# Optimization experiments

Hardware: AMD Instinct MI355X
Metric: run time of the kernel (lower is better)

The kernel has to match this reference:

```python
import jax, jax.numpy as jnp
import numpy as np

B, H, T, D = 2, 16, 2048, 64
R1, R2 = 4, 8


def setup_inputs() -> dict:
    key = jax.random.key(0)
    ks = jax.random.split(key, 7)
    return {
        "q": jax.random.normal(ks[0], (B, H, T, D), dtype=jnp.float32),
        "k": jax.random.normal(ks[1], (B, H, T, D), dtype=jnp.float32),
        "v": jax.random.normal(ks[2], (B, H, T, D), dtype=jnp.float32),
        "W_q": jax.random.normal(ks[3], (H, D, R1 * R2), dtype=jnp.float32) / np.sqrt(D),
        "W_k": jax.random.normal(ks[4], (H, D, R1 * R2), dtype=jnp.float32) / np.sqrt(D),
        "core1": jax.random.normal(ks[5], (H, R1), dtype=jnp.float32),
        "core2": jax.random.normal(ks[6], (H, R2), dtype=jnp.float32),
    }


def reference(q, k, v, W_q, W_k, core1, core2):
    """Kronecker low-rank (LSR) causal attention.

    scores[b,h,m,n] = (1/sqrt(R1*R2)) * sum_r kron[h,r] * (q@W_q)[b,h,m,r] * (k@W_k)[b,h,n,r]
    where kron[h] = core1[h] (x) core2[h]  (per-head Kronecker product).
    """
    Hh, r1 = core1.shape
    r2 = core2.shape[1]
    # per-head Kronecker core vector: (H, R1*R2)
    kron = (core1[:, :, None] * core2[:, None, :]).reshape(Hh, r1 * r2)
    scale = 1.0 / jnp.sqrt(jnp.float32(r1 * r2))
    # low-rank projections, rank R = R1*R2
    q_lr = jnp.einsum("bhtd,hdr->bhtr", q, W_q) * kron[None, :, None, :]  # [B,H,T,R]
    k_lr = jnp.einsum("bhtd,hdr->bhtr", k, W_k)                            # [B,H,T,R]
    scores = jnp.einsum("bhmr,bhnr->bhmn", q_lr, k_lr) * scale             # [B,H,T,T]
    t = q.shape[2]
    causal = jnp.tril(jnp.ones((t, t), dtype=bool))
    scores = jnp.where(causal[None, None], scores, -jnp.inf)
    p = jax.nn.softmax(scores, axis=-1)
    return jnp.einsum("bhmn,bhnd->bhmd", p, v)
```

## Files before the change

kernel.cpp:

```cpp
#include <hip/hip_runtime.h>

typedef _Float16 f16;
typedef _Float16 f16x2 __attribute__((ext_vector_type(2)));
typedef _Float16 f16x4 __attribute__((ext_vector_type(4)));
typedef _Float16 f16x8 __attribute__((ext_vector_type(8)));
typedef float    f32x4 __attribute__((ext_vector_type(4)));
typedef float    f32x16 __attribute__((ext_vector_type(16)));

constexpr int B_ = 2, H_ = 16, T_ = 2048, D_ = 64, R_ = 32, NT = 32;

__device__ __forceinline__ f32x4 mfma16(f16x8 a, f16x8 b, f32x4 c) {
  return __builtin_amdgcn_mfma_f32_16x16x32_f16(a, b, c, 0, 0, 0);
}
__device__ __forceinline__ f32x16 mfma32(f16x8 a, f16x8 b, f32x16 c) {
  return __builtin_amdgcn_mfma_f32_32x32x16_f16(a, b, c, 0, 0, 0);
}
__device__ __forceinline__ void ld_lds16(const void* g, void* l) {
  __builtin_amdgcn_global_load_lds(
      (const __attribute__((address_space(1))) unsigned int*)g,
      (__attribute__((address_space(3))) unsigned int*)l, 16, 0, 0);
}

__global__ __launch_bounds__(256) void proj_kernel(
    const float* __restrict__ q, const float* __restrict__ k, const float* __restrict__ v,
    const float* __restrict__ Wq, const float* __restrict__ Wk,
    const float* __restrict__ c1, const float* __restrict__ c2,
    f16* __restrict__ qlr, f16* __restrict__ klr, f16* __restrict__ vt)
{
  __shared__ float sv[64 * 65];

  const int tid = threadIdx.x, w = tid >> 6, lane = tid & 63;
  const int l15 = lane & 15, l4 = lane >> 4;
  const int bh = blockIdx.x >> 5, h = bh & (H_ - 1);
  const int t0 = (blockIdx.x & 31) * 64;

  const float* vb = v + ((size_t)bh * T_ + t0) * D_;
  float4 vld[4];
#pragma unroll
  for (int it = 0; it < 4; ++it) vld[it] = ((const float4*)vb)[it * 256 + tid];

  const int m = t0 + 16 * w + l15;
  const float* qr = q + ((size_t)bh * T_ + m) * D_;
  const float* kr = k + ((size_t)bh * T_ + m) * D_;
  f16x8 aq[2], ak[2];
#pragma unroll
  for (int kc = 0; kc < 2; ++kc) {
    float4 x0 = *(const float4*)(qr + kc * 32 + 8 * l4);
    float4 x1 = *(const float4*)(qr + kc * 32 + 8 * l4 + 4);
    float4 y0 = *(const float4*)(kr + kc * 32 + 8 * l4);
    float4 y1 = *(const float4*)(kr + kc * 32 + 8 * l4 + 4);
    f16x8 A, K;
    A[0]=(f16)x0.x; A[1]=(f16)x0.y; A[2]=(f16)x0.z; A[3]=(f16)x0.w;
    A[4]=(f16)x1.x; A[5]=(f16)x1.y; A[6]=(f16)x1.z; A[7]=(f16)x1.w;
    K[0]=(f16)y0.x; K[1]=(f16)y0.y; K[2]=(f16)y0.z; K[3]=(f16)y0.w;
    K[4]=(f16)y1.x; K[5]=(f16)y1.y; K[6]=(f16)y1.z; K[7]=(f16)y1.w;
    aq[kc] = A; ak[kc] = K;
  }

  const float* Wqh = Wq + (size_t)h * D_ * R_;
  const float* Wkh = Wk + (size_t)h * D_ * R_;
  f16x8 bq[2][2], bk[2][2];
#pragma unroll
  for (int kc = 0; kc < 2; ++kc)
#pragma unroll
    for (int nt = 0; nt < 2; ++nt) {
      const int r = 16 * nt + l15;
      f16x8 q8, k8;
#pragma unroll
      for (int j2 = 0; j2 < 8; ++j2) {
        const int d = kc * 32 + 8 * l4 + j2;
        q8[j2] = (f16)Wqh[d * R_ + r];
        k8[j2] = (f16)Wkh[d * R_ + r];
      }
      bq[kc][nt] = q8; bk[kc][nt] = k8;
    }

#pragma unroll
  for (int it = 0; it < 4; ++it) {
    const int i4 = it * 256 + tid, t = i4 >> 4, dq = (i4 & 15) * 4;
    sv[t * 65 + dq    ] = vld[it].x;
    sv[t * 65 + dq + 1] = vld[it].y;
    sv[t * 65 + dq + 2] = vld[it].z;
    sv[t * 65 + dq + 3] = vld[it].w;
  }

  const f32x4 z4 = {0.f, 0.f, 0.f, 0.f};
#pragma unroll
  for (int nt = 0; nt < 2; ++nt) {
    f32x4 accq = mfma16(aq[0], bq[0][nt], z4);
    accq = mfma16(aq[1], bq[1][nt], accq);
    f32x4 acck = mfma16(ak[0], bk[0][nt], z4);
    acck = mfma16(ak[1], bk[1][nt], acck);
    const int r = 16 * nt + l15;
    const float scl = c1[h * 4 + (r >> 3)] * c2[h * 8 + (r & 7)] *
                      (0.17677669529663687f * 1.4426950408889634f);
#pragma unroll
    for (int i = 0; i < 4; ++i) {
      const size_t row = (size_t)bh * T_ + t0 + 16 * w + 4 * l4 + i;
      qlr[row * R_ + r] = (f16)(accq[i] * scl);
      klr[row * R_ + r] = (f16)acck[i];
    }
  }

  __syncthreads();
#pragma unroll
  for (int it = 0; it < 8; ++it) {
    const int idx = it * 256 + tid, d = idx >> 5, t = (idx & 31) * 2;
    const float f0 = sv[t * 65 + d], f1 = sv[t * 65 + 65 + d];
    f16x2 pr; pr[0] = (f16)f0; pr[1] = (f16)f1;
    const int sw = ((((t >> 3) ^ (d & 7)) << 3) | (t & 7));
    *(f16x2*)(vt + ((size_t)bh * D_ + d) * T_ + t0 + sw) = pr;
  }
}

__global__ __launch_bounds__(128) void attn_kernel(
    const f16* __restrict__ qlr, const f16* __restrict__ klr,
    const f16* __restrict__ vt, float* __restrict__ out)
{
  __shared__ __align__(16) f16 s_k[64 * 32];
  __shared__ __align__(16) f16 s_vt[64 * 64];
  __shared__ __align__(16) f16 s_p[2][32 * 64];

  const int tid = threadIdx.x, w = tid >> 6, lane = tid & 63;
  const int l15 = lane & 15, l4 = lane >> 4, l31 = lane & 31, hh = lane >> 5;
  const int bh = blockIdx.x & 31;
  const int mt = 31 - (blockIdx.x >> 5);
  const int m0 = mt * 64;

  const f16x8 aq0 = *(const f16x8*)(qlr + ((size_t)bh * T_ + m0 + 32 * w + l15) * R_ + 8 * l4);
  const f16x8 aq1 = *(const f16x8*)(qlr + ((size_t)bh * T_ + m0 + 32 * w + 16 + l15) * R_ + 8 * l4);

  const f16* kb = klr + (size_t)bh * T_ * R_;
  const f16* vb = vt + (size_t)bh * D_ * T_;

  f32x16 oacc[2];
#pragma unroll
  for (int c = 0; c < 2; ++c)
#pragma unroll
    for (int e = 0; e < 16; ++e) oacc[c][e] = 0.f;
  float mi0 = -1e30f, mi1 = -1e30f, li0 = 0.f, li1 = 0.f;
  const f32x4 z4 = {0.f, 0.f, 0.f, 0.f};

  for (int j = 0; j <= mt; ++j) {
    const int n0 = 64 * j;
    __syncthreads();
#pragma unroll
    for (int e = 0; e < 2; ++e)
      ld_lds16((const char*)kb + (size_t)n0 * 64 + (2 * w + e) * 1024 + lane * 16,
               (char*)s_k + (2 * w + e) * 1024);
#pragma unroll
    for (int e = 0; e < 4; ++e) {
      const int d0 = w * 32 + e * 8;
      ld_lds16((const char*)vb + ((size_t)(d0 + (lane >> 3)) * T_ + n0) * 2 + (lane & 7) * 16,
               (char*)s_vt + d0 * 128);
    }
    __syncthreads();

    f32x4 sc[4][2];
#pragma unroll
    for (int ns = 0; ns < 4; ++ns) {
      f16x8 akf = *(const f16x8*)&s_k[(16 * ns + l15) * 32 + 8 * l4];
      sc[ns][0] = mfma16(akf, aq0, z4);
      sc[ns][1] = mfma16(akf, aq1, z4);
    }
    if (j == mt) {
      const int lim0 = 32 * w + l15;
#pragma unroll
      for (int ns = 0; ns < 4; ++ns) {
        const int nb = 16 * ns + 4 * l4;
#pragma unroll
        for (int i = 0; i < 4; ++i) {
          if (nb + i > lim0)      sc[ns][0][i] = -1e30f;
          if (nb + i > lim0 + 16) sc[ns][1][i] = -1e30f;
        }
      }
    }

    float rm0 = -1e30f, rm1 = -1e30f;
#pragma unroll
    for (int ns = 0; ns < 4; ++ns)
#pragma unroll
      for (int i = 0; i < 4; ++i) {
        rm0 = fmaxf(rm0, sc[ns][0][i]);
        rm1 = fmaxf(rm1, sc[ns][1][i]);
      }
    rm0 = fmaxf(rm0, __shfl_xor(rm0, 16)); rm0 = fmaxf(rm0, __shfl_xor(rm0, 32));
    rm1 = fmaxf(rm1, __shfl_xor(rm1, 16)); rm1 = fmaxf(rm1, __shfl_xor(rm1, 32));
    const float mn0 = fmaxf(mi0, rm0), mn1 = fmaxf(mi1, rm1);
    const float a0 = exp2f(mi0 - mn0), a1 = exp2f(mi1 - mn1);
    float rs0 = 0.f, rs1 = 0.f;
#pragma unroll
    for (int ns = 0; ns < 4; ++ns) {
      f16x4 p0v, p1v;
#pragma unroll
      for (int i = 0; i < 4; ++i) {
        const float p0 = exp2f(sc[ns][0][i] - mn0);
        const float p1 = exp2f(sc[ns][1][i] - mn1);
        rs0 += p0; rs1 += p1;
        p0v[i] = (f16)p0; p1v[i] = (f16)p1;
      }
      const int col = ((((2 * ns + (l4 >> 1)) ^ (l15 & 7)) << 3) | (4 * (l4 & 1)));
      *(f16x4*)&s_p[w][l15 * 64 + col]        = p0v;
      *(f16x4*)&s_p[w][(16 + l15) * 64 + col] = p1v;
    }
    rs0 += __shfl_xor(rs0, 16); rs0 += __shfl_xor(rs0, 32);
    rs1 += __shfl_xor(rs1, 16); rs1 += __shfl_xor(rs1, 32);
    li0 = li0 * a0 + rs0; li1 = li1 * a1 + rs1;
    mi0 = mn0; mi1 = mn1;
    const float aPV = (lane & 16) ? a1 : a0;
#pragma unroll
    for (int c = 0; c < 2; ++c) oacc[c] *= aPV;

#pragma unroll
    for (int kc = 0; kc < 4; ++kc) {
      const int u = (2 * kc + hh) ^ (l31 & 7);
      f16x8 bp = *(const f16x8*)&s_p[w][l31 * 64 + u * 8];
#pragma unroll
      for (int c = 0; c < 2; ++c) {
        f16x8 av = *(const f16x8*)&s_vt[(32 * c + l31) * 64 + u * 8];
        oacc[c] = mfma32(av, bp, oacc[c]);
      }
    }
  }

  const float invl = 1.f / ((lane & 16) ? li1 : li0);
  float* ob = out + ((size_t)bh * T_ + m0 + 32 * w + l31) * D_;
#pragma unroll
  for (int c = 0; c < 2; ++c)
#pragma unroll
    for (int g = 0; g < 4; ++g) {
      f32x4 o;
#pragma unroll
      for (int e = 0; e < 4; ++e) o[e] = oacc[c][4 * g + e] * invl;
      *(f32x4*)(ob + 32 * c + 8 * g + 4 * hh) = o;
    }
}

extern "C" void kernel_launch(void* const* d_in, const int* in_sizes, int n_in,
                              void* d_out, int out_size, void* d_ws, size_t ws_size,
                              hipStream_t stream) {
  const float* q  = (const float*)d_in[0];
  const float* k  = (const float*)d_in[1];
  const float* v  = (const float*)d_in[2];
  const float* Wq = (const float*)d_in[3];
  const float* Wk = (const float*)d_in[4];
  const float* c1 = (const float*)d_in[5];
  const float* c2 = (const float*)d_in[6];
  float* out = (float*)d_out;

  f16* qlr = (f16*)d_ws;
  f16* klr = qlr + (size_t)B_ * H_ * T_ * R_;
  f16* vt  = klr + (size_t)B_ * H_ * T_ * R_;

  proj_kernel<<<B_ * H_ * NT, 256, 0, stream>>>(q, k, v, Wq, Wk, c1, c2, qlr, klr, vt);
  attn_kernel<<<B_ * H_ * NT, 128, 0, stream>>>(qlr, klr, vt, out);
}
```

Measured before the change: 162.0 us.

## Split causal attention KV loop across two blocks and merge partial results

Each query tile's KV loop is split into NS interleaved slices handled by separate blocks. Every block writes an fp16 partial output plus its row max and sum to workspace, and a new merge kernel combines them into the final fp32 output. The aim is to double the grid of 1024 small blocks for better occupancy and to balance the long causal tiles. The cost is extra workspace traffic, a third kernel launch, and fp16 rounding of the partial outputs. The split only applies if the workspace is large enough; otherwise NS is 1 and results pass through fp16 as well.

```diff
diff --git a/kernel.cpp b/kernel.cpp
--- a/kernel.cpp
+++ b/kernel.cpp
@@ -8,6 +8,7 @@
 typedef float    f32x16 __attribute__((ext_vector_type(16)));
 
 constexpr int B_ = 2, H_ = 16, T_ = 2048, D_ = 64, R_ = 32, NT = 32;
+constexpr int NROW = B_ * H_ * T_;
 
 __device__ __forceinline__ f32x4 mfma16(f16x8 a, f16x8 b, f32x4 c) {
   return __builtin_amdgcn_mfma_f32_16x16x32_f16(a, b, c, 0, 0, 0);
@@ -115,7 +116,8 @@
 
 __global__ __launch_bounds__(128) void attn_kernel(
     const f16* __restrict__ qlr, const f16* __restrict__ klr,
-    const f16* __restrict__ vt, float* __restrict__ out)
+    const f16* __restrict__ vt, f16* __restrict__ On, float2* __restrict__ ml,
+    const int NS)
 {
   __shared__ __align__(16) f16 s_k[64 * 32];
   __shared__ __align__(16) f16 s_vt[64 * 64];
@@ -124,7 +126,9 @@
   const int tid = threadIdx.x, w = tid >> 6, lane = tid & 63;
   const int l15 = lane & 15, l4 = lane >> 4, l31 = lane & 31, hh = lane >> 5;
   const int bh = blockIdx.x & 31;
-  const int mt = 31 - (blockIdx.x >> 5);
+  const int rest = blockIdx.x >> 5;
+  const int mt = 31 - ((NS == 2) ? (rest >> 1) : rest);
+  const int s  = rest & (NS - 1);
   const int m0 = mt * 64;
 
   const f16x8 aq0 = *(const f16x8*)(qlr + ((size_t)bh * T_ + m0 + 32 * w + l15) * R_ + 8 * l4);
@@ -141,7 +145,7 @@
   float mi0 = -1e30f, mi1 = -1e30f, li0 = 0.f, li1 = 0.f;
   const f32x4 z4 = {0.f, 0.f, 0.f, 0.f};
 
-  for (int j = 0; j <= mt; ++j) {
+  for (int j = s; j <= mt; j += NS) {
     const int n0 = 64 * j;
     __syncthreads();
 #pragma unroll
@@ -223,17 +227,55 @@
     }
   }
 
-  const float invl = 1.f / ((lane & 16) ? li1 : li0);
-  float* ob = out + ((size_t)bh * T_ + m0 + 32 * w + l31) * D_;
+  const float myl = (lane & 16) ? li1 : li0;
+  const float invl = myl > 0.f ? 1.f / myl : 0.f;
+  f16* ob = On + (((size_t)s * 32 + bh) * T_ + m0 + 32 * w + l31) * D_;
 #pragma unroll
   for (int c = 0; c < 2; ++c)
 #pragma unroll
     for (int g = 0; g < 4; ++g) {
-      f32x4 o;
-#pragma unroll
-      for (int e = 0; e < 4; ++e) o[e] = oacc[c][4 * g + e] * invl;
-      *(f32x4*)(ob + 32 * c + 8 * g + 4 * hh) = o;
-    }
+      f16x4 o;
+#pragma unroll
+      for (int e = 0; e < 4; ++e) o[e] = (f16)(oacc[c][4 * g + e] * invl);
+      *(f16x4*)(ob + 32 * c + 8 * g + 4 * hh) = o;
+    }
+  if (l4 < 2) {
+    float2 mlv;
+    mlv.x = l4 ? mi1 : mi0;
+    mlv.y = l4 ? li1 : li0;
+    ml[((size_t)s * 32 + bh) * T_ + m0 + 32 * w + 16 * l4 + l15] = mlv;
+  }
+}
+
+__global__ __launch_bounds__(256) void merge_kernel(
+    const f16* __restrict__ On, const float2* __restrict__ ml,
+    float* __restrict__ out, const int NS)
+{
+  const int row = blockIdx.x * 32 + (threadIdx.x >> 3);
+  const int d0 = (threadIdx.x & 7) * 8;
+  const f16x8 o0 = *(const f16x8*)(On + (size_t)row * 64 + d0);
+  float res[8];
+  if (NS == 2) {
+    const float2 a = ml[row];
+    const float2 b = ml[NROW + row];
+    const f16x8 o1 = *(const f16x8*)(On + ((size_t)NROW + row) * 64 + d0);
+    const float ms = fmaxf(a.x, b.x);
+    const float w0 = exp2f(a.x - ms) * a.y;
+    const float w1 = exp2f(b.x - ms) * b.y;
+    const float inv = 1.f / (w0 + w1);
+    const float c0 = w0 * inv, c1 = w1 * inv;
+#pragma unroll
+    for (int e = 0; e < 8; ++e) res[e] = c0 * (float)o0[e] + c1 * (float)o1[e];
+  } else {
+#pragma unroll
+    for (int e = 0; e < 8; ++e) res[e] = (float)o0[e];
+  }
+  float* ob = out + (size_t)row * 64 + d0;
+  f32x4 r0, r1;
+#pragma unroll
+  for (int e = 0; e < 4; ++e) { r0[e] = res[e]; r1[e] = res[4 + e]; }
+  *(f32x4*)ob = r0;
+  *(f32x4*)(ob + 4) = r1;
 }
 
 extern "C" void kernel_launch(void* const* d_in, const int* in_sizes, int n_in,
@@ -251,7 +293,12 @@
   f16* qlr = (f16*)d_ws;
   f16* klr = qlr + (size_t)B_ * H_ * T_ * R_;
   f16* vt  = klr + (size_t)B_ * H_ * T_ * R_;
+  f16* On  = vt + (size_t)B_ * H_ * T_ * D_;
+  float2* ml = (float2*)(On + (size_t)2 * NROW * D_);
+
+  const int NS = (ws_size >= ((size_t)33 * 1024 * 1024 + (1 << 20))) ? 2 : 1;
 
   proj_kernel<<<B_ * H_ * NT, 256, 0, stream>>>(q, k, v, Wq, Wk, c1, c2, qlr, klr, vt);
-  attn_kernel<<<B_ * H_ * NT, 128, 0, stream>>>(qlr, klr, vt, out);
-}
+  attn_kernel<<<B_ * H_ * NT * NS, 128, 0, stream>>>(qlr, klr, vt, On, ml, NS);
+  merge_kernel<<<NROW / 32, 256, 0, stream>>>(On, ml, out, NS);
+}
```

Result: faster. 153.7 us (-5.1%).
